# Kernel optimization log

Measured on AMD Instinct MI355X. Metric: run time of the kernel, lower is better.

Reference implementation:

```python
import jax, jax.numpy as jnp
import numpy as np

H = 4
N = 50000
D_IN = 128
D_MODEL = 256
NCLASS = 40
B_S = 1
BH = B_S * H
LN_EPS = 1e-5


def sparse_perm_1D(indices, values, feats, n, bh):
    """Batched sparse (bh,n,n) @ dense (bh,n,d): gather -> scale -> segment-sum scatter."""
    gathered = feats[indices[0], indices[2]]              # (nnz, d)
    contrib = values[:, None] * gathered                   # (nnz, d)
    seg = indices[0] * n + indices[1]                      # (nnz,)
    out = jax.ops.segment_sum(contrib, seg, num_segments=bh * n)
    return out.reshape(bh, n, -1)


def layer_norm(x, gamma, beta):
    mu = jnp.mean(x, axis=-1, keepdims=True)
    var = jnp.var(x, axis=-1, keepdims=True)
    return (x - mu) * jax.lax.rsqrt(var + LN_EPS) * gamma + beta


def setup_inputs() -> dict:
    key = jax.random.key(0)
    k1, k2, k3, k4, k5, k6, k7 = jax.random.split(key, 7)
    # per-(batch*head) permutation sigma: nonzero at (b, i, sigma_b(i))
    perm_keys = jax.random.split(k1, BH)
    sigma = jax.vmap(lambda k: jax.random.permutation(k, N))(perm_keys)  # (BH, N)
    b_idx = jnp.repeat(jnp.arange(BH), N)
    row_idx = jnp.tile(jnp.arange(N), BH)
    col_idx = sigma.reshape(-1)
    perm_indices = jnp.stack([b_idx, row_idx, col_idx], axis=0).astype(jnp.int32)  # (3, BH*N)
    perm_values = jax.random.uniform(k2, (BH * N,), dtype=jnp.float32)
    features = jax.random.normal(k3, (B_S, N, D_IN), dtype=jnp.float32)
    appd = jax.random.normal(k4, (B_S, N, D_IN), dtype=jnp.float32)
    # parameters
    w_scale_in = 1.0 / np.sqrt(2 * D_IN)
    W_in = jax.random.uniform(k5, (2 * D_IN, D_MODEL), dtype=jnp.float32, minval=-w_scale_in, maxval=w_scale_in)
    b_in = jnp.zeros((D_MODEL,), dtype=jnp.float32)
    ln_gamma = jnp.ones((D_MODEL * H,), dtype=jnp.float32)
    ln_beta = jnp.zeros((D_MODEL * H,), dtype=jnp.float32)
    w_scale_h = 1.0 / np.sqrt(D_MODEL * H)
    W_head = jax.random.uniform(k6, (D_MODEL * H, NCLASS), dtype=jnp.float32, minval=-w_scale_h, maxval=w_scale_h)
    b_head = jax.random.uniform(k7, (NCLASS,), dtype=jnp.float32, minval=-w_scale_h, maxval=w_scale_h)
    return {"perm_indices": perm_indices, "perm_values": perm_values,
            "features": features, "appd": appd,
            "W_in": W_in, "b_in": b_in,
            "ln_gamma": ln_gamma, "ln_beta": ln_beta,
            "W_head": W_head, "b_head": b_head}


def reference(perm_indices, perm_values, features, appd, W_in, b_in, ln_gamma, ln_beta, W_head, b_head):
    # concat auxiliary features, replicate per head: (B_S,N,2*D_IN) -> (BH,N,2*D_IN)
    feat = jnp.concatenate([features, appd], axis=-1)
    feat = jnp.broadcast_to(feat[:, None], (B_S, H, N, 2 * D_IN)).reshape(BH, N, 2 * D_IN)
    # permute rows: perm @ feat
    x = sparse_perm_1D(perm_indices, perm_values, feat, N, BH)
    # ff_in + relu (dropout is identity at eval)
    x = jax.nn.relu(x @ W_in + b_in)                       # (BH, N, D_MODEL)
    # nlayers == nblocks == 0: compress/uncompress loops are empty
    # inverse permutation: perm^T @ x (swap row/col indices)
    idx_t = jnp.stack([perm_indices[0], perm_indices[2], perm_indices[1]], axis=0)
    y = sparse_perm_1D(idx_t, perm_values, x, N, BH)       # (BH, N, D_MODEL)
    # (B_S,H,N,D) -> (B_S,N,H*D)
    y = y.reshape(B_S, H, N, D_MODEL).transpose(0, 2, 1, 3).reshape(B_S, N, H * D_MODEL)
    y = layer_norm(y, ln_gamma, ln_beta)
    return y @ W_head + b_head                             # (B_S, N, NCLASS)
```

## Files before the change

kernel.cpp:

```cpp
#include <hip/hip_runtime.h>
#include <hip/hip_bf16.h>

#define NROW 50000
#define DIN 128
#define DM 256
#define HH 4
#define NC 40
#define BHN 200000
#define NBLK 1563

typedef float f32x4 __attribute__((ext_vector_type(4)));
typedef short bf16x8 __attribute__((ext_vector_type(8)));

__device__ __forceinline__ unsigned short f2bf(float x) {
    unsigned int u = __float_as_uint(x);
    u += 0x7fffu + ((u >> 16) & 1u);
    return (unsigned short)(u >> 16);
}

__device__ __forceinline__ unsigned int pk2(float lo, float hi) {
    __hip_bfloat162 h = __float22bfloat162_rn(make_float2(lo, hi));
    return *(unsigned int*)&h;
}

__device__ __forceinline__ float bf2f(unsigned short s) {
    return __uint_as_float(((unsigned int)s) << 16);
}

__global__ __launch_bounds__(256) void k_prep(const int* __restrict__ pi,
                                              const float* __restrict__ pv,
                                              const float* __restrict__ Win,
                                              const float* __restrict__ Wh,
                                              const float* __restrict__ gamma,
                                              const float* __restrict__ beta,
                                              const float* __restrict__ bh,
                                              float* __restrict__ vcol,
                                              unsigned short* __restrict__ Wpk,
                                              unsigned short* __restrict__ Wgpk,
                                              float* __restrict__ bias2) {
    const int bid = blockIdx.x, tid = threadIdx.x;
    if (bid < 782) {
        int k = bid * 256 + tid;
        if (k < BHN) {
            int b = (k >= 150000) ? 3 : (k >= 100000) ? 2 : (k >= 50000) ? 1 : 0;
            int col = pi[2 * BHN + k];
            vcol[b * NROW + col] = pv[k];
        }
    } else if (bid < 798) {
        int base = (bid - 782) * 512;
        #pragma unroll
        for (int q = 0; q < 2; ++q) {
            int s = base + q * 256 + tid;
            int ln = s & 63;
            int t  = (s >> 6) & 15;
            int kc = s >> 10;
            int n  = t * 16 + (ln & 15);
            int kb = kc * 32 + ((ln >> 4) << 3);
            union { unsigned int ui[4]; uint4 v4; } u;
            #pragma unroll
            for (int jj = 0; jj < 4; ++jj)
                u.ui[jj] = pk2(Win[(kb + 2 * jj) * DM + n], Win[(kb + 2 * jj + 1) * DM + n]);
            *(uint4*)&Wpk[s * 8] = u.v4;
        }
    } else if (bid < 810) {
        int base = (bid - 798) * 512;
        #pragma unroll
        for (int q = 0; q < 2; ++q) {
            int s = base + q * 256 + tid;
            int ln = s & 63;
            int u6 = s >> 6;
            int t  = u6 % 3;
            int v6 = u6 / 3;
            int kc = v6 & 7;
            int h  = v6 >> 3;
            int c  = t * 16 + (ln & 15);
            int d0 = h * 256 + kc * 32 + ((ln >> 4) << 3);
            union { unsigned int ui[4]; uint4 v4; } u;
            if (c < NC) {
                #pragma unroll
                for (int jj = 0; jj < 4; ++jj)
                    u.ui[jj] = pk2(gamma[d0 + 2 * jj] * Wh[(d0 + 2 * jj) * NC + c],
                                   gamma[d0 + 2 * jj + 1] * Wh[(d0 + 2 * jj + 1) * NC + c]);
            } else {
                u.v4 = make_uint4(0u, 0u, 0u, 0u);
            }
            *(uint4*)&Wgpk[s * 8] = u.v4;
        }
    } else {
        __shared__ float red[256];
        int c = bid - 810;
        float sacc = 0.f;
        #pragma unroll
        for (int q = 0; q < 4; ++q) {
            int d = tid + 256 * q;
            sacc = fmaf(beta[d], Wh[d * NC + c], sacc);
        }
        red[tid] = sacc;
        __syncthreads();
        for (int st = 128; st > 0; st >>= 1) {
            if (tid < st) red[tid] += red[tid + st];
            __syncthreads();
        }
        if (tid == 0) bias2[c] = bh[c] + red[0];
    }
}

__global__ __launch_bounds__(64, 2) void k_fused(
    const float* __restrict__ feats, const float* __restrict__ appd,
    const unsigned short* __restrict__ Wpk,
    const unsigned short* __restrict__ Wgpk,
    const float* __restrict__ vcol,
    const float* __restrict__ b_in,
    const float* __restrict__ bias2,
    float* __restrict__ out)
{
    __shared__ __align__(16) unsigned short Gb[32 * 264];
    __shared__ float rsS[32], nmS[32];

    const int tid = threadIdx.x;
    const int quad = tid >> 4;
    const int lr = tid & 15;
    const int j0 = blockIdx.x * 32;

    const int ar0 = min(j0 + lr, NROW - 1);
    const int ar1 = min(j0 + 16 + lr, NROW - 1);

    const f32x4 zero4 = {0.f, 0.f, 0.f, 0.f};
    f32x4 accG[2][16];
    #pragma unroll
    for (int rt = 0; rt < 2; ++rt)
        #pragma unroll
        for (int t = 0; t < 16; ++t) accG[rt][t] = zero4;

    #pragma unroll
    for (int kc = 0; kc < 8; ++kc) {
        const float* src = (kc < 4) ? feats : appd;
        const int ko = (kc & 3) * 32 + quad * 8;
        union { unsigned int ui[4]; bf16x8 v; } a0, a1;
        {
            float4 x0 = *(const float4*)&src[(size_t)ar0 * DIN + ko];
            float4 x1 = *(const float4*)&src[(size_t)ar0 * DIN + ko + 4];
            a0.ui[0] = pk2(x0.x, x0.y); a0.ui[1] = pk2(x0.z, x0.w);
            a0.ui[2] = pk2(x1.x, x1.y); a0.ui[3] = pk2(x1.z, x1.w);
            float4 y0 = *(const float4*)&src[(size_t)ar1 * DIN + ko];
            float4 y1 = *(const float4*)&src[(size_t)ar1 * DIN + ko + 4];
            a1.ui[0] = pk2(y0.x, y0.y); a1.ui[1] = pk2(y0.z, y0.w);
            a1.ui[2] = pk2(y1.x, y1.y); a1.ui[3] = pk2(y1.z, y1.w);
        }
        #pragma unroll
        for (int t = 0; t < 16; ++t) {
            bf16x8 bf = *(const bf16x8*)&Wpk[(size_t)(((kc * 16 + t) << 6) + tid) * 8];
            accG[0][t] = __builtin_amdgcn_mfma_f32_16x16x32_bf16(a0.v, bf, accG[0][t], 0, 0, 0);
            accG[1][t] = __builtin_amdgcn_mfma_f32_16x16x32_bf16(a1.v, bf, accG[1][t], 0, 0, 0);
        }
    }

    float bt[16];
    #pragma unroll
    for (int t = 0; t < 16; ++t) bt[t] = b_in[t * 16 + lr];

    #pragma unroll
    for (int rt = 0; rt < 2; ++rt) {
        float vhh[HH][4];
        #pragma unroll
        for (int h = 0; h < HH; ++h)
            #pragma unroll
            for (int rg = 0; rg < 4; ++rg)
                vhh[h][rg] = vcol[h * NROW + min(j0 + rt * 16 + quad * 4 + rg, NROW - 1)];

        float s[4] = {0.f, 0.f, 0.f, 0.f}, ss[4] = {0.f, 0.f, 0.f, 0.f};
        #pragma unroll
        for (int t = 0; t < 16; ++t)
            #pragma unroll
            for (int rg = 0; rg < 4; ++rg) {
                float gg = accG[rt][t][rg];
                Gb[(rt * 16 + quad * 4 + rg) * 264 + t * 16 + lr] = f2bf(gg);
                #pragma unroll
                for (int h = 0; h < HH; ++h) {
                    float v = vhh[h][rg];
                    float y = v * fmaxf(fmaf(v, gg, bt[t]), 0.f);
                    s[rg] += y;
                    ss[rg] = fmaf(y, y, ss[rg]);
                }
            }
        #pragma unroll
        for (int m = 1; m <= 8; m <<= 1)
            #pragma unroll
            for (int rg = 0; rg < 4; ++rg) {
                s[rg] += __shfl_xor(s[rg], m);
                ss[rg] += __shfl_xor(ss[rg], m);
            }
        if (lr == 0) {
            #pragma unroll
            for (int rg = 0; rg < 4; ++rg) {
                float mm = s[rg] * (1.f / 1024.f);
                float var = ss[rg] * (1.f / 1024.f) - mm * mm;
                float r_ = rsqrtf(var + 1e-5f);
                rsS[rt * 16 + quad * 4 + rg] = r_;
                nmS[rt * 16 + quad * 4 + rg] = -mm * r_;
            }
        }
    }
    __syncthreads();

    float vm[HH][2];
    #pragma unroll
    for (int h = 0; h < HH; ++h) {
        vm[h][0] = vcol[h * NROW + min(j0 + lr, NROW - 1)];
        vm[h][1] = vcol[h * NROW + min(j0 + 16 + lr, NROW - 1)];
    }
    const float rs0 = rsS[lr], nm0 = nmS[lr];
    const float rs1 = rsS[16 + lr], nm1 = nmS[16 + lr];

    f32x4 accO[2][3];
    #pragma unroll
    for (int rt = 0; rt < 2; ++rt)
        #pragma unroll
        for (int t = 0; t < 3; ++t) accO[rt][t] = zero4;

    #pragma unroll
    for (int kc = 0; kc < 8; ++kc) {
        bf16x8 gf0 = *(const bf16x8*)&Gb[lr * 264 + kc * 32 + quad * 8];
        bf16x8 gf1 = *(const bf16x8*)&Gb[(16 + lr) * 264 + kc * 32 + quad * 8];
        float4 bA = *(const float4*)&b_in[kc * 32 + quad * 8];
        float4 bB = *(const float4*)&b_in[kc * 32 + quad * 8 + 4];
        float bb[8] = {bA.x, bA.y, bA.z, bA.w, bB.x, bB.y, bB.z, bB.w};
        float g0[8], g1[8];
        #pragma unroll
        for (int j = 0; j < 8; ++j) {
            g0[j] = bf2f((unsigned short)gf0[j]);
            g1[j] = bf2f((unsigned short)gf1[j]);
        }
        #pragma unroll
        for (int h = 0; h < HH; ++h) {
            union { unsigned int ui[4]; bf16x8 v; } u0, u1;
            #pragma unroll
            for (int jj = 0; jj < 4; ++jj) {
                float ya = vm[h][0] * fmaxf(fmaf(vm[h][0], g0[2 * jj], bb[2 * jj]), 0.f);
                float yb = vm[h][0] * fmaxf(fmaf(vm[h][0], g0[2 * jj + 1], bb[2 * jj + 1]), 0.f);
                u0.ui[jj] = pk2(fmaf(ya, rs0, nm0), fmaf(yb, rs0, nm0));
                float yc = vm[h][1] * fmaxf(fmaf(vm[h][1], g1[2 * jj], bb[2 * jj]), 0.f);
                float yd = vm[h][1] * fmaxf(fmaf(vm[h][1], g1[2 * jj + 1], bb[2 * jj + 1]), 0.f);
                u1.ui[jj] = pk2(fmaf(yc, rs1, nm1), fmaf(yd, rs1, nm1));
            }
            #pragma unroll
            for (int t = 0; t < 3; ++t) {
                bf16x8 wf = *(const bf16x8*)&Wgpk[(size_t)(((((h * 8 + kc) * 3 + t) << 6) + tid)) * 8];
                accO[0][t] = __builtin_amdgcn_mfma_f32_16x16x32_bf16(u0.v, wf, accO[0][t], 0, 0, 0);
                accO[1][t] = __builtin_amdgcn_mfma_f32_16x16x32_bf16(u1.v, wf, accO[1][t], 0, 0, 0);
            }
        }
    }

    float b2[3];
    #pragma unroll
    for (int t = 0; t < 3; ++t) {
        int c = t * 16 + lr;
        b2[t] = (c < NC) ? bias2[c] : 0.f;
    }
    #pragma unroll
    for (int rt = 0; rt < 2; ++rt)
        #pragma unroll
        for (int t = 0; t < 3; ++t) {
            int c = t * 16 + lr;
            if (c < NC) {
                #pragma unroll
                for (int rg = 0; rg < 4; ++rg) {
                    int row = j0 + rt * 16 + quad * 4 + rg;
                    if (row < NROW)
                        out[(size_t)row * NC + c] = accO[rt][t][rg] + b2[t];
                }
            }
        }
}

extern "C" void kernel_launch(void* const* d_in, const int* in_sizes, int n_in,
                              void* d_out, int out_size, void* d_ws, size_t ws_size,
                              hipStream_t stream) {
    const int*   pi    = (const int*)d_in[0];
    const float* pv    = (const float*)d_in[1];
    const float* feats = (const float*)d_in[2];
    const float* appd  = (const float*)d_in[3];
    const float* Win   = (const float*)d_in[4];
    const float* b_in  = (const float*)d_in[5];
    const float* gamma = (const float*)d_in[6];
    const float* beta  = (const float*)d_in[7];
    const float* Wh    = (const float*)d_in[8];
    const float* bh    = (const float*)d_in[9];
    float* out = (float*)d_out;

    char* w = (char*)d_ws;
    float*          vcolW  = (float*)w;
    unsigned short* WpkW   = (unsigned short*)(w + 800000);
    unsigned short* WgpkW  = (unsigned short*)(w + 931072);
    float*          bias2W = (float*)(w + 1029376);

    k_prep<<<850, 256, 0, stream>>>(pi, pv, Win, Wh, gamma, beta, bh, vcolW, WpkW, WgpkW, bias2W);
    k_fused<<<NBLK, 64, 0, stream>>>(feats, appd, WpkW, WgpkW, vcolW, b_in, bias2W, out);
}
```

Before: 153.5 us.

## Factor per-head scale and LayerNorm affine out of head GEMM epilogue

Moves the per-head value scaling and the LayerNorm normalize step out of the A-operand construction of the second GEMM. Each head now gets its own accumulator, and the epilogue combines them as rs*(sum_h v_h*acc_h) - rs*mean*colsum(gamma*W) + bias2. The colsum is precomputed in the prep kernel. The first GEMM is split into two column chunks of eight tiles each to lower peak accumulator registers, but the second GEMM's accumulators grow fourfold (24 f32x4), which raises register pressure and risks spills or lower occupancy.

```diff
diff --git a/kernel.cpp b/kernel.cpp
--- a/kernel.cpp
+++ b/kernel.cpp
@@ -37,7 +37,8 @@
                                               float* __restrict__ vcol,
                                               unsigned short* __restrict__ Wpk,
                                               unsigned short* __restrict__ Wgpk,
-                                              float* __restrict__ bias2) {
+                                              float* __restrict__ bias2,
+                                              float* __restrict__ cs) {
     const int bid = blockIdx.x, tid = threadIdx.x;
     if (bid < 782) {
         int k = bid * 256 + tid;
@@ -87,21 +88,23 @@
             *(uint4*)&Wgpk[s * 8] = u.v4;
         }
     } else {
-        __shared__ float red[256];
+        __shared__ float red[256], red2[256];
         int c = bid - 810;
-        float sacc = 0.f;
+        float sb = 0.f, sc = 0.f;
         #pragma unroll
         for (int q = 0; q < 4; ++q) {
             int d = tid + 256 * q;
-            sacc = fmaf(beta[d], Wh[d * NC + c], sacc);
-        }
-        red[tid] = sacc;
+            float w = Wh[d * NC + c];
+            sb = fmaf(beta[d], w, sb);
+            sc = fmaf(gamma[d], w, sc);
+        }
+        red[tid] = sb; red2[tid] = sc;
         __syncthreads();
         for (int st = 128; st > 0; st >>= 1) {
-            if (tid < st) red[tid] += red[tid + st];
+            if (tid < st) { red[tid] += red[tid + st]; red2[tid] += red2[tid + st]; }
             __syncthreads();
         }
-        if (tid == 0) bias2[c] = bh[c] + red[0];
+        if (tid == 0) { bias2[c] = bh[c] + red[0]; cs[c] = red2[0]; }
     }
 }
 
@@ -112,10 +115,11 @@
     const float* __restrict__ vcol,
     const float* __restrict__ b_in,
     const float* __restrict__ bias2,
+    const float* __restrict__ cs,
     float* __restrict__ out)
 {
     __shared__ __align__(16) unsigned short Gb[32 * 264];
-    __shared__ float rsS[32], nmS[32];
+    __shared__ float rsS[32], rmS[32];
 
     const int tid = threadIdx.x;
     const int quad = tid >> 4;
@@ -125,81 +129,89 @@
     const int ar0 = min(j0 + lr, NROW - 1);
     const int ar1 = min(j0 + 16 + lr, NROW - 1);
 
+    float vhh[2][HH][4];
+    #pragma unroll
+    for (int rt = 0; rt < 2; ++rt)
+        #pragma unroll
+        for (int h = 0; h < HH; ++h)
+            #pragma unroll
+            for (int rg = 0; rg < 4; ++rg)
+                vhh[rt][h][rg] = vcol[h * NROW + min(j0 + rt * 16 + quad * 4 + rg, NROW - 1)];
+
     const f32x4 zero4 = {0.f, 0.f, 0.f, 0.f};
-    f32x4 accG[2][16];
-    #pragma unroll
-    for (int rt = 0; rt < 2; ++rt)
-        #pragma unroll
-        for (int t = 0; t < 16; ++t) accG[rt][t] = zero4;
-
-    #pragma unroll
-    for (int kc = 0; kc < 8; ++kc) {
-        const float* src = (kc < 4) ? feats : appd;
-        const int ko = (kc & 3) * 32 + quad * 8;
-        union { unsigned int ui[4]; bf16x8 v; } a0, a1;
-        {
-            float4 x0 = *(const float4*)&src[(size_t)ar0 * DIN + ko];
-            float4 x1 = *(const float4*)&src[(size_t)ar0 * DIN + ko + 4];
-            a0.ui[0] = pk2(x0.x, x0.y); a0.ui[1] = pk2(x0.z, x0.w);
-            a0.ui[2] = pk2(x1.x, x1.y); a0.ui[3] = pk2(x1.z, x1.w);
-            float4 y0 = *(const float4*)&src[(size_t)ar1 * DIN + ko];
-            float4 y1 = *(const float4*)&src[(size_t)ar1 * DIN + ko + 4];
-            a1.ui[0] = pk2(y0.x, y0.y); a1.ui[1] = pk2(y0.z, y0.w);
-            a1.ui[2] = pk2(y1.x, y1.y); a1.ui[3] = pk2(y1.z, y1.w);
-        }
-        #pragma unroll
-        for (int t = 0; t < 16; ++t) {
-            bf16x8 bf = *(const bf16x8*)&Wpk[(size_t)(((kc * 16 + t) << 6) + tid) * 8];
-            accG[0][t] = __builtin_amdgcn_mfma_f32_16x16x32_bf16(a0.v, bf, accG[0][t], 0, 0, 0);
-            accG[1][t] = __builtin_amdgcn_mfma_f32_16x16x32_bf16(a1.v, bf, accG[1][t], 0, 0, 0);
-        }
-    }
-
-    float bt[16];
-    #pragma unroll
-    for (int t = 0; t < 16; ++t) bt[t] = b_in[t * 16 + lr];
-
-    #pragma unroll
-    for (int rt = 0; rt < 2; ++rt) {
-        float vhh[HH][4];
-        #pragma unroll
-        for (int h = 0; h < HH; ++h)
-            #pragma unroll
-            for (int rg = 0; rg < 4; ++rg)
-                vhh[h][rg] = vcol[h * NROW + min(j0 + rt * 16 + quad * 4 + rg, NROW - 1)];
-
-        float s[4] = {0.f, 0.f, 0.f, 0.f}, ss[4] = {0.f, 0.f, 0.f, 0.f};
-        #pragma unroll
-        for (int t = 0; t < 16; ++t)
+    float s_[2][4] = {}, ss_[2][4] = {};
+
+    #pragma unroll
+    for (int ch = 0; ch < 2; ++ch) {
+        f32x4 accG[2][8];
+        #pragma unroll
+        for (int rt = 0; rt < 2; ++rt)
+            #pragma unroll
+            for (int t = 0; t < 8; ++t) accG[rt][t] = zero4;
+
+        #pragma unroll
+        for (int kc = 0; kc < 8; ++kc) {
+            const float* src = (kc < 4) ? feats : appd;
+            const int ko = (kc & 3) * 32 + quad * 8;
+            union { unsigned int ui[4]; bf16x8 v; } a0, a1;
+            {
+                float4 x0 = *(const float4*)&src[(size_t)ar0 * DIN + ko];
+                float4 x1 = *(const float4*)&src[(size_t)ar0 * DIN + ko + 4];
+                a0.ui[0] = pk2(x0.x, x0.y); a0.ui[1] = pk2(x0.z, x0.w);
+                a0.ui[2] = pk2(x1.x, x1.y); a0.ui[3] = pk2(x1.z, x1.w);
+                float4 y0 = *(const float4*)&src[(size_t)ar1 * DIN + ko];
+                float4 y1 = *(const float4*)&src[(size_t)ar1 * DIN + ko + 4];
+                a1.ui[0] = pk2(y0.x, y0.y); a1.ui[1] = pk2(y0.z, y0.w);
+                a1.ui[2] = pk2(y1.x, y1.y); a1.ui[3] = pk2(y1.z, y1.w);
+            }
+            #pragma unroll
+            for (int t = 0; t < 8; ++t) {
+                bf16x8 bf = *(const bf16x8*)&Wpk[(size_t)(((kc * 16 + ch * 8 + t) << 6) + tid) * 8];
+                accG[0][t] = __builtin_amdgcn_mfma_f32_16x16x32_bf16(a0.v, bf, accG[0][t], 0, 0, 0);
+                accG[1][t] = __builtin_amdgcn_mfma_f32_16x16x32_bf16(a1.v, bf, accG[1][t], 0, 0, 0);
+            }
+        }
+        float bt[8];
+        #pragma unroll
+        for (int t = 0; t < 8; ++t) bt[t] = b_in[(ch * 8 + t) * 16 + lr];
+        #pragma unroll
+        for (int rt = 0; rt < 2; ++rt)
+            #pragma unroll
+            for (int t = 0; t < 8; ++t)
+                #pragma unroll
+                for (int rg = 0; rg < 4; ++rg) {
+                    float gg = accG[rt][t][rg];
+                    Gb[(rt * 16 + quad * 4 + rg) * 264 + (ch * 8 + t) * 16 + lr] = f2bf(gg);
+                    #pragma unroll
+                    for (int h = 0; h < HH; ++h) {
+                        float v = vhh[rt][h][rg];
+                        float y = v * fmaxf(fmaf(v, gg, bt[t]), 0.f);
+                        s_[rt][rg] += y;
+                        ss_[rt][rg] = fmaf(y, y, ss_[rt][rg]);
+                    }
+                }
+    }
+
+    #pragma unroll
+    for (int m = 1; m <= 8; m <<= 1)
+        #pragma unroll
+        for (int rt = 0; rt < 2; ++rt)
             #pragma unroll
             for (int rg = 0; rg < 4; ++rg) {
-                float gg = accG[rt][t][rg];
-                Gb[(rt * 16 + quad * 4 + rg) * 264 + t * 16 + lr] = f2bf(gg);
-                #pragma unroll
-                for (int h = 0; h < HH; ++h) {
-                    float v = vhh[h][rg];
-                    float y = v * fmaxf(fmaf(v, gg, bt[t]), 0.f);
-                    s[rg] += y;
-                    ss[rg] = fmaf(y, y, ss[rg]);
-                }
-            }
-        #pragma unroll
-        for (int m = 1; m <= 8; m <<= 1)
+                s_[rt][rg] += __shfl_xor(s_[rt][rg], m);
+                ss_[rt][rg] += __shfl_xor(ss_[rt][rg], m);
+            }
+    if (lr == 0) {
+        #pragma unroll
+        for (int rt = 0; rt < 2; ++rt)
             #pragma unroll
             for (int rg = 0; rg < 4; ++rg) {
-                s[rg] += __shfl_xor(s[rg], m);
-                ss[rg] += __shfl_xor(ss[rg], m);
-            }
-        if (lr == 0) {
-            #pragma unroll
-            for (int rg = 0; rg < 4; ++rg) {
-                float mm = s[rg] * (1.f / 1024.f);
-                float var = ss[rg] * (1.f / 1024.f) - mm * mm;
+                float mm = s_[rt][rg] * (1.f / 1024.f);
+                float var = ss_[rt][rg] * (1.f / 1024.f) - mm * mm;
                 float r_ = rsqrtf(var + 1e-5f);
                 rsS[rt * 16 + quad * 4 + rg] = r_;
-                nmS[rt * 16 + quad * 4 + rg] = -mm * r_;
-            }
-        }
+                rmS[rt * 16 + quad * 4 + rg] = r_ * mm;
+            }
     }
     __syncthreads();
 
@@ -209,14 +221,14 @@
         vm[h][0] = vcol[h * NROW + min(j0 + lr, NROW - 1)];
         vm[h][1] = vcol[h * NROW + min(j0 + 16 + lr, NROW - 1)];
     }
-    const float rs0 = rsS[lr], nm0 = nmS[lr];
-    const float rs1 = rsS[16 + lr], nm1 = nmS[16 + lr];
-
-    f32x4 accO[2][3];
-    #pragma unroll
-    for (int rt = 0; rt < 2; ++rt)
-        #pragma unroll
-        for (int t = 0; t < 3; ++t) accO[rt][t] = zero4;
+
+    f32x4 accO[HH][2][3];
+    #pragma unroll
+    for (int h = 0; h < HH; ++h)
+        #pragma unroll
+        for (int rt = 0; rt < 2; ++rt)
+            #pragma unroll
+            for (int t = 0; t < 3; ++t) accO[h][rt][t] = zero4;
 
     #pragma unroll
     for (int kc = 0; kc < 8; ++kc) {
@@ -236,39 +248,48 @@
             union { unsigned int ui[4]; bf16x8 v; } u0, u1;
             #pragma unroll
             for (int jj = 0; jj < 4; ++jj) {
-                float ya = vm[h][0] * fmaxf(fmaf(vm[h][0], g0[2 * jj], bb[2 * jj]), 0.f);
-                float yb = vm[h][0] * fmaxf(fmaf(vm[h][0], g0[2 * jj + 1], bb[2 * jj + 1]), 0.f);
-                u0.ui[jj] = pk2(fmaf(ya, rs0, nm0), fmaf(yb, rs0, nm0));
-                float yc = vm[h][1] * fmaxf(fmaf(vm[h][1], g1[2 * jj], bb[2 * jj]), 0.f);
-                float yd = vm[h][1] * fmaxf(fmaf(vm[h][1], g1[2 * jj + 1], bb[2 * jj + 1]), 0.f);
-                u1.ui[jj] = pk2(fmaf(yc, rs1, nm1), fmaf(yd, rs1, nm1));
+                float ya = fmaxf(fmaf(vm[h][0], g0[2 * jj], bb[2 * jj]), 0.f);
+                float yb = fmaxf(fmaf(vm[h][0], g0[2 * jj + 1], bb[2 * jj + 1]), 0.f);
+                u0.ui[jj] = pk2(ya, yb);
+                float yc = fmaxf(fmaf(vm[h][1], g1[2 * jj], bb[2 * jj]), 0.f);
+                float yd = fmaxf(fmaf(vm[h][1], g1[2 * jj + 1], bb[2 * jj + 1]), 0.f);
+                u1.ui[jj] = pk2(yc, yd);
             }
             #pragma unroll
             for (int t = 0; t < 3; ++t) {
-                bf16x8 wf = *(const bf16x8*)&Wgpk[(size_t)(((((h * 8 + kc) * 3 + t) << 6) + tid)) * 8];
-                accO[0][t] = __builtin_amdgcn_mfma_f32_16x16x32_bf16(u0.v, wf, accO[0][t], 0, 0, 0);
-                accO[1][t] = __builtin_amdgcn_mfma_f32_16x16x32_bf16(u1.v, wf, accO[1][t], 0, 0, 0);
-            }
-        }
-    }
-
-    float b2[3];
+                bf16x8 wf = *(const bf16x8*)&Wgpk[(size_t)((((h * 8 + kc) * 3 + t) << 6) + tid) * 8];
+                accO[h][0][t] = __builtin_amdgcn_mfma_f32_16x16x32_bf16(u0.v, wf, accO[h][0][t], 0, 0, 0);
+                accO[h][1][t] = __builtin_amdgcn_mfma_f32_16x16x32_bf16(u1.v, wf, accO[h][1][t], 0, 0, 0);
+            }
+        }
+    }
+
+    float ct[3], b2[3];
     #pragma unroll
     for (int t = 0; t < 3; ++t) {
         int c = t * 16 + lr;
+        ct[t] = (c < NC) ? cs[c] : 0.f;
         b2[t] = (c < NC) ? bias2[c] : 0.f;
     }
     #pragma unroll
     for (int rt = 0; rt < 2; ++rt)
         #pragma unroll
-        for (int t = 0; t < 3; ++t) {
-            int c = t * 16 + lr;
-            if (c < NC) {
+        for (int rg = 0; rg < 4; ++rg) {
+            int rr = rt * 16 + quad * 4 + rg;
+            int row = j0 + rr;
+            if (row < NROW) {
+                float rsv = rsS[rr], rmv = rmS[rr];
                 #pragma unroll
-                for (int rg = 0; rg < 4; ++rg) {
-                    int row = j0 + rt * 16 + quad * 4 + rg;
-                    if (row < NROW)
-                        out[(size_t)row * NC + c] = accO[rt][t][rg] + b2[t];
+                for (int t = 0; t < 3; ++t) {
+                    int c = t * 16 + lr;
+                    if (c < NC) {
+                        float raw = vhh[rt][0][rg] * accO[0][rt][t][rg];
+                        raw = fmaf(vhh[rt][1][rg], accO[1][rt][t][rg], raw);
+                        raw = fmaf(vhh[rt][2][rg], accO[2][rt][t][rg], raw);
+                        raw = fmaf(vhh[rt][3][rg], accO[3][rt][t][rg], raw);
+                        float base = fmaf(-rmv, ct[t], b2[t]);
+                        out[(size_t)row * NC + c] = fmaf(rsv, raw, base);
+                    }
                 }
             }
         }
@@ -294,7 +315,8 @@
     unsigned short* WpkW   = (unsigned short*)(w + 800000);
     unsigned short* WgpkW  = (unsigned short*)(w + 931072);
     float*          bias2W = (float*)(w + 1029376);
-
-    k_prep<<<850, 256, 0, stream>>>(pi, pv, Win, Wh, gamma, beta, bh, vcolW, WpkW, WgpkW, bias2W);
-    k_fused<<<NBLK, 64, 0, stream>>>(feats, appd, WpkW, WgpkW, vcolW, b_in, bias2W, out);
-}
+    float*          csW    = (float*)(w + 1029536);
+
+    k_prep<<<850, 256, 0, stream>>>(pi, pv, Win, Wh, gamma, beta, bh, vcolW, WpkW, WgpkW, bias2W, csW);
+    k_fused<<<NBLK, 64, 0, stream>>>(feats, appd, WpkW, WgpkW, vcolW, b_in, bias2W, csW, out);
+}
```

New measurement: 158.2 us. +3.0%, slower.
